# Optimization experiments

Measured on AMD Instinct MI355X. Metric: run time of the kernel, lower is better.

## Reference

```python
import jax, jax.numpy as jnp
import numpy as np

HID = 512
HEADS = 8
HD = HID // HEADS  # 64


def setup_inputs() -> dict:
    key = jax.random.key(0)
    ks = jax.random.split(key, 16)
    B, LQ, LK = 2, 384, 384
    s_in = 1.0 / np.sqrt(HID)
    s_hd = 1.0 / np.sqrt(HD)
    return {
        "query": jax.random.normal(ks[0], (B, LQ, HID), jnp.float32),
        "key":   jax.random.normal(ks[1], (B, LK, HID), jnp.float32),
        "value": jax.random.normal(ks[2], (B, LK, HID), jnp.float32),
        # linear weights stored as (in, out) so y = x @ W + b
        "Wq": jax.random.uniform(ks[3], (HID, HID), jnp.float32, -s_in, s_in),
        "bq": jnp.zeros((HID,), jnp.float32),
        "Wk": jax.random.uniform(ks[4], (HID, HID), jnp.float32, -s_in, s_in),
        "bk": jnp.zeros((HID,), jnp.float32),
        "Wv": jax.random.uniform(ks[5], (HID, HID), jnp.float32, -s_in, s_in),
        "bv": jnp.zeros((HID,), jnp.float32),
        "Ww": jax.random.uniform(ks[6], (HD, HD), jnp.float32, -s_hd, s_hd),
        "bw": jnp.zeros((HD,), jnp.float32),
        "Wu": jax.random.uniform(ks[7], (HD, HD), jnp.float32, -s_hd, s_hd),
        "bu": jnp.zeros((HD,), jnp.float32),
        "vv": jax.random.uniform(ks[8], (HD,), jnp.float32, -s_hd, s_hd),
        "Wo": jax.random.uniform(ks[9], (HID, HID), jnp.float32, -s_in, s_in),
        "bo": jnp.zeros((HID,), jnp.float32),
    }


def reference(query, key, value, Wq, bq, Wk, bk, Wv, bv, Ww, bw, Wu, bu, vv, Wo, bo):
    B, LQ, _ = query.shape
    LK = key.shape[1]
    scale = jnp.sqrt(jnp.asarray(HD, query.dtype))

    def split_heads(x, L):
        return x.reshape(B, L, HEADS, HD).transpose(0, 2, 1, 3)  # [B,H,L,hd]

    Q = split_heads(query @ Wq + bq, LQ)
    K = split_heads(key @ Wk + bk, LK)
    V = split_heads(value @ Wv + bv, LK)

    qW = Q @ Ww + bw            # [B,H,Lq,hd]
    kU = K @ Wu + bu            # [B,H,Lk,hd]
    # additive energy: tanh(W(Q)+U(K)) . vv  -> [B,H,Lq,Lk]
    e = jnp.tanh(qW[:, :, :, None, :] + kU[:, :, None, :, :])  # [B,H,Lq,Lk,hd]
    energy = jnp.einsum('bhqkd,d->bhqk', e, vv) / scale

    attention = jax.nn.softmax(energy, axis=-1)
    x = jnp.einsum('bhqk,bhkd->bhqd', attention, V)
    x = x.transpose(0, 2, 1, 3).reshape(B, LQ, HID)
    x = x @ Wo + bo
    return (x, attention)
```

## Files before the change

kernel.cpp:

```cpp
#include <hip/hip_runtime.h>

#define HID 512
#define HEADS 8
#define HD 64
#define BATCH 2
#define SEQ 384
#define MROWS (BATCH * SEQ)
#define APACK_S8 (48 * 32 * 64)
#define BPACK_S8 (32 * 32 * 64)

#define C1 2.8853900817779268f
#define SSCL 0.18033688011112043f

typedef __attribute__((ext_vector_type(8))) short s8v;
typedef __attribute__((ext_vector_type(4))) float f4v;

__device__ __forceinline__ unsigned short bf16_rne(float x) {
    union { float f; unsigned u; } v; v.f = x;
    unsigned r = v.u + 0x7FFFu + ((v.u >> 16) & 1u);
    return (unsigned short)(r >> 16);
}
__device__ __forceinline__ float bf16_val(unsigned short h) {
    union { float f; unsigned u; } v; v.u = ((unsigned)h) << 16; return v.f;
}

__device__ __forceinline__ void pack_a_one(const float* __restrict__ src,
                                           s8v* __restrict__ dst, int rem)
{
    int g = rem & 63, m = rem >> 6;
    const float4* sp = (const float4*)(src + (size_t)m * HID + g * 8);
    float4 v0 = sp[0], v1 = sp[1];
    float vals[8] = {v0.x, v0.y, v0.z, v0.w, v1.x, v1.y, v1.z, v1.w};
    s8v hi, lo;
    #pragma unroll
    for (int j = 0; j < 8; ++j) {
        unsigned short h = bf16_rne(vals[j]);
        hi[j] = (short)h;
        lo[j] = (short)bf16_rne(vals[j] - bf16_val(h));
    }
    int mt = m >> 4, kt = g >> 2;
    int lanei = (m & 15) | ((g & 3) << 4);
    size_t base = ((size_t)mt * 32) * 64 + lanei;
    dst[base + (size_t)kt * 64]        = hi;
    dst[base + (size_t)(16 + kt) * 64] = lo;
}

__device__ __forceinline__ void pack_w_store(s8v* __restrict__ dst,
                                             const float vals[8], int kg, int n)
{
    s8v hi, lo;
    #pragma unroll
    for (int j = 0; j < 8; ++j) {
        unsigned short h = bf16_rne(vals[j]);
        hi[j] = (short)h;
        lo[j] = (short)bf16_rne(vals[j] - bf16_val(h));
    }
    int nt = n >> 4, kt = kg >> 2;
    int lanei = (n & 15) | ((kg & 3) << 4);
    size_t base = ((size_t)nt * 32) * 64 + lanei;
    dst[base + (size_t)kt * 64]        = hi;
    dst[base + (size_t)(16 + kt) * 64] = lo;
}

__device__ __forceinline__ void pack_w_one(const float* __restrict__ W,
                                           s8v* __restrict__ dst, int rem)
{
    int kg = rem >> 9, n = rem & 511;
    float vals[8];
    #pragma unroll
    for (int j = 0; j < 8; ++j)
        vals[j] = W[(size_t)(kg * 8 + j) * HID + n];
    pack_w_store(dst, vals, kg, n);
}

__device__ __forceinline__ void fold_pack_w_one(const float* __restrict__ Wbig,
                                                const float* __restrict__ Wsmall,
                                                s8v* __restrict__ dst, int rem)
{
    int kg = __builtin_amdgcn_readfirstlane(rem >> 9);
    int n  = rem & 511;
    int h  = __builtin_amdgcn_readfirstlane(n >> 6);
    int d  = n & 63;
    const float* wr = Wbig + (size_t)(kg * 8) * HID + h * HD;
    float acc[8] = {0.f, 0.f, 0.f, 0.f, 0.f, 0.f, 0.f, 0.f};
    #pragma unroll 8
    for (int t = 0; t < 64; ++t) {
        float wv = Wsmall[t * 64 + d];
        #pragma unroll
        for (int j = 0; j < 8; ++j)
            acc[j] = fmaf(wr[(size_t)j * HID + t], wv, acc[j]);
    }
    pack_w_store(dst, acc, kg, n);
}

__global__ __launch_bounds__(256) void pack_all_kernel(
    const float* __restrict__ q, const float* __restrict__ k, const float* __restrict__ v,
    const float* __restrict__ Wq, const float* __restrict__ bq,
    const float* __restrict__ Wk, const float* __restrict__ bk,
    const float* __restrict__ Wv, const float* __restrict__ Wo,
    const float* __restrict__ Ww, const float* __restrict__ bw,
    const float* __restrict__ Wu, const float* __restrict__ bu,
    const float* __restrict__ vv,
    s8v* __restrict__ Aq, s8v* __restrict__ Ak, s8v* __restrict__ Av,
    s8v* __restrict__ Bq, s8v* __restrict__ Bk, s8v* __restrict__ Bv, s8v* __restrict__ Bo,
    float* __restrict__ bqe, float* __restrict__ bke, float* __restrict__ vv2)
{
    int bx = blockIdx.x, tid = threadIdx.x;
    if (bx < 576) {
        int p = bx / 192;
        int rem = (bx % 192) * 256 + tid;
        const float* src = (p == 0) ? q : (p == 1) ? k : v;
        s8v* dst = (p == 0) ? Aq : (p == 1) ? Ak : Av;
        pack_a_one(src, dst, rem);
    } else if (bx < 704) {
        pack_w_one(Wv, Bv, (bx - 576) * 256 + tid);
    } else if (bx < 832) {
        pack_w_one(Wo, Bo, (bx - 704) * 256 + tid);
    } else if (bx < 960) {
        fold_pack_w_one(Wq, Ww, Bq, (bx - 832) * 256 + tid);
    } else if (bx < 1088) {
        fold_pack_w_one(Wk, Wu, Bk, (bx - 960) * 256 + tid);
    } else {
        for (int i = tid; i < 1088; i += 256) {
            if (i < 512) {
                int h = i >> 6, j = i & 63;
                float s = bw[j];
                for (int t = 0; t < 64; ++t) s = fmaf(bq[h * 64 + t], Ww[t * 64 + j], s);
                bqe[i] = s;
            } else if (i < 1024) {
                int n = i - 512, h = n >> 6, j = n & 63;
                float s = bu[j];
                for (int t = 0; t < 64; ++t) s = fmaf(bk[h * 64 + t], Wu[t * 64 + j], s);
                bke[n] = s;
            } else {
                vv2[i - 1024] = -2.0f * vv[i - 1024];
            }
        }
    }
}

struct Frag { s8v ah0, al0, ah1, al1, bh0, bl0, bh1, bl1; };

__device__ __forceinline__ void load_frag(Frag& f,
    const s8v* __restrict__ a0, const s8v* __restrict__ a1,
    const s8v* __restrict__ b0, const s8v* __restrict__ b1, int kt)
{
    int oh = kt * 64, ol = (16 + kt) * 64;
    f.ah0 = a0[oh]; f.al0 = a0[ol];
    f.ah1 = a1[oh]; f.al1 = a1[ol];
    f.bh0 = b0[oh]; f.bl0 = b0[ol];
    f.bh1 = b1[oh]; f.bl1 = b1[ol];
}

__device__ __forceinline__ void compute_frag(f4v& acc00, f4v& acc01,
                                             f4v& acc10, f4v& acc11, const Frag& f)
{
    acc00 = __builtin_amdgcn_mfma_f32_16x16x32_bf16(f.ah0, f.bh0, acc00, 0, 0, 0);
    acc01 = __builtin_amdgcn_mfma_f32_16x16x32_bf16(f.ah0, f.bh1, acc01, 0, 0, 0);
    acc10 = __builtin_amdgcn_mfma_f32_16x16x32_bf16(f.ah1, f.bh0, acc10, 0, 0, 0);
    acc11 = __builtin_amdgcn_mfma_f32_16x16x32_bf16(f.ah1, f.bh1, acc11, 0, 0, 0);
    acc00 = __builtin_amdgcn_mfma_f32_16x16x32_bf16(f.ah0, f.bl0, acc00, 0, 0, 0);
    acc01 = __builtin_amdgcn_mfma_f32_16x16x32_bf16(f.ah0, f.bl1, acc01, 0, 0, 0);
    acc10 = __builtin_amdgcn_mfma_f32_16x16x32_bf16(f.ah1, f.bl0, acc10, 0, 0, 0);
    acc11 = __builtin_amdgcn_mfma_f32_16x16x32_bf16(f.ah1, f.bl1, acc11, 0, 0, 0);
    acc00 = __builtin_amdgcn_mfma_f32_16x16x32_bf16(f.al0, f.bh0, acc00, 0, 0, 0);
    acc01 = __builtin_amdgcn_mfma_f32_16x16x32_bf16(f.al0, f.bh1, acc01, 0, 0, 0);
    acc10 = __builtin_amdgcn_mfma_f32_16x16x32_bf16(f.al1, f.bh0, acc10, 0, 0, 0);
    acc11 = __builtin_amdgcn_mfma_f32_16x16x32_bf16(f.al1, f.bh1, acc11, 0, 0, 0);
}

template <int MODE>
__device__ __forceinline__ void mfma_gemm_body(
    const s8v* __restrict__ Ap, const s8v* __restrict__ Bp,
    const float* __restrict__ bias, float* __restrict__ out,
    int mt0, int nt0)
{
    __shared__ f4v red[4][4][64];

    int tid  = threadIdx.x;
    int wave = __builtin_amdgcn_readfirstlane(tid >> 6);
    int lane = tid & 63;

    const s8v* a0p = Ap + (size_t)(mt0 * 32) * 64 + lane;
    const s8v* a1p = a0p + (size_t)32 * 64;
    const s8v* b0p = Bp + (size_t)(nt0 * 32) * 64 + lane;
    const s8v* b1p = b0p + (size_t)32 * 64;

    f4v acc00 = {0.f, 0.f, 0.f, 0.f};
    f4v acc01 = {0.f, 0.f, 0.f, 0.f};
    f4v acc10 = {0.f, 0.f, 0.f, 0.f};
    f4v acc11 = {0.f, 0.f, 0.f, 0.f};

    int kt0 = wave * 4;
    Frag X, Y;
    load_frag(X, a0p, a1p, b0p, b1p, kt0);
    load_frag(Y, a0p, a1p, b0p, b1p, kt0 + 1);
    compute_frag(acc00, acc01, acc10, acc11, X);
    load_frag(X, a0p, a1p, b0p, b1p, kt0 + 2);
    compute_frag(acc00, acc01, acc10, acc11, Y);
    load_frag(Y, a0p, a1p, b0p, b1p, kt0 + 3);
    compute_frag(acc00, acc01, acc10, acc11, X);
    compute_frag(acc00, acc01, acc10, acc11, Y);

    red[wave][0][lane] = acc00;
    red[wave][1][lane] = acc01;
    red[wave][2][lane] = acc10;
    red[wave][3][lane] = acc11;
    __syncthreads();

    f4v s = red[0][wave][lane] + red[1][wave][lane]
          + red[2][wave][lane] + red[3][wave][lane];

    int quad = lane >> 4, c16 = lane & 15;
    int R0 = mt0 * 16 + quad * 4 + (wave >> 1) * 16;
    int C  = nt0 * 16 + c16 + (wave & 1) * 16;
    float biasC = bias[C];

    #pragma unroll
    for (int r = 0; r < 4; ++r) {
        float yy = s[r] + biasC;
        if (MODE != 0) yy = __builtin_amdgcn_exp2f(C1 * yy);
        if (MODE == 2) {
            int ROW = R0 + r;
            int b2 = ROW / SEQ, kk = ROW - b2 * SEQ;
            int hh = C >> 6, dd = C & 63;
            out[(((size_t)((b2 * 8 + hh) * 16 + (dd >> 2)) * SEQ + kk) << 2)
                + (dd & 3)] = yy;
        } else {
            out[(size_t)(R0 + r) * HID + C] = yy;
        }
    }
}

__global__ __launch_bounds__(256) void proj3_mfma_kernel(
    const s8v* __restrict__ Aq, const s8v* __restrict__ Ak, const s8v* __restrict__ Av,
    const s8v* __restrict__ Bq, const s8v* __restrict__ Bk, const s8v* __restrict__ Bv,
    const float* __restrict__ bqe, const float* __restrict__ bke, const float* __restrict__ bv,
    float* __restrict__ Eq, float* __restrict__ Ek4, float* __restrict__ V)
{
    int p = blockIdx.z;
    int mt0 = blockIdx.x * 2, nt0 = blockIdx.y * 2;
    if (p == 0)      mfma_gemm_body<1>(Aq, Bq, bqe, Eq,  mt0, nt0);
    else if (p == 1) mfma_gemm_body<2>(Ak, Bk, bke, Ek4, mt0, nt0);
    else             mfma_gemm_body<0>(Av, Bv, bv,  V,   mt0, nt0);
}

__global__ __launch_bounds__(256) void out_mfma_kernel(
    const s8v* __restrict__ Ax, const s8v* __restrict__ Bo,
    const float* __restrict__ bo, float* __restrict__ out)
{
    mfma_gemm_body<0>(Ax, Bo, bo, out, blockIdx.x * 2, blockIdx.y * 2);
}

__global__ __launch_bounds__(256, 4) void attn_kernel(
    const float* __restrict__ Eq, const float* __restrict__ Ek4,
    const float* __restrict__ V, const float* __restrict__ vv2,
    float* __restrict__ attnOut, s8v* __restrict__ Ax)
{
    __shared__ float2 aP[4][SEQ];

    int blk = blockIdx.x;
    int xcd = blk & 7, slot = blk >> 3;
    int part = slot / 48, qblk = slot % 48;
    int bh = xcd * 2 + part;
    int b = bh >> 3, h = bh & 7;
    int tid = threadIdx.x;
    int wave = __builtin_amdgcn_readfirstlane(tid >> 6);
    int lane = tid & 63;
    int q0 = qblk * 8 + wave * 2, q1 = q0 + 1;

    const float* eq0 = Eq + (size_t)(b * SEQ + q0) * HID + h * HD;
    const float* eq1 = eq0 + HID;
    const float4* ekbase = (const float4*)Ek4 + (size_t)bh * 16 * SEQ + lane;

    float e0[6], e1[6];
    #pragma unroll
    for (int t = 0; t < 6; ++t) { e0[t] = 0.f; e1[t] = 0.f; }

    #pragma unroll 1
    for (int cc = 0; cc < 4; ++cc) {
        int c = (cc + wave) & 3;
        float g0[16], g1[16], w[16];
        #pragma unroll
        for (int j = 0; j < 16; ++j) {
            g0[j] = eq0[c * 16 + j];
            g1[j] = eq1[c * 16 + j];
            w[j]  = vv2[c * 16 + j];
        }
        const float4* ekc = ekbase + (size_t)c * 4 * SEQ;
        float4 k0 = ekc[0 * SEQ], k1 = ekc[1 * SEQ];
        float4 k2 = ekc[2 * SEQ], k3 = ekc[3 * SEQ];
        #pragma unroll
        for (int kt = 0; kt < 6; ++kt) {
            float4 n0, n1, n2, n3;
            if (kt < 5) {
                const float4* np = ekc + (kt + 1) * 64;
                n0 = np[0 * SEQ]; n1 = np[1 * SEQ];
                n2 = np[2 * SEQ]; n3 = np[3 * SEQ];
            }
            float r0 = e0[kt], r1 = e1[kt];
            #define EN(J, KV)                                                      \
            {                                                                      \
                float t0 = __builtin_amdgcn_rcpf(fmaf(g0[J], (KV), 1.f));          \
                float t1 = __builtin_amdgcn_rcpf(fmaf(g1[J], (KV), 1.f));          \
                r0 = fmaf(w[J], t0, r0);                                           \
                r1 = fmaf(w[J], t1, r1);                                           \
            }
            EN(0,  k0.x) EN(1,  k0.y) EN(2,  k0.z) EN(3,  k0.w)
            EN(4,  k1.x) EN(5,  k1.y) EN(6,  k1.z) EN(7,  k1.w)
            EN(8,  k2.x) EN(9,  k2.y) EN(10, k2.z) EN(11, k2.w)
            EN(12, k3.x) EN(13, k3.y) EN(14, k3.z) EN(15, k3.w)
            #undef EN
            e0[kt] = r0; e1[kt] = r1;
            k0 = n0; k1 = n1; k2 = n2; k3 = n3;
        }
    }

    int ko = lane >> 4, d4p = lane & 15;
    const float4* vb = (const float4*)&V[(size_t)b * SEQ * HID + h * HD + d4p * 4];
    float4 vpre[8];
    #pragma unroll
    for (int i = 0; i < 8; ++i)
        vpre[i] = vb[(size_t)(ko + i * 4) * (HID / 4)];

    float m0 = e0[0], m1 = e1[0];
    #pragma unroll
    for (int t = 1; t < 6; ++t) { m0 = fmaxf(m0, e0[t]); m1 = fmaxf(m1, e1[t]); }
    #pragma unroll
    for (int off = 1; off < 64; off <<= 1) {
        m0 = fmaxf(m0, __shfl_xor(m0, off));
        m1 = fmaxf(m1, __shfl_xor(m1, off));
    }
    float a0[6], a1[6], s0 = 0.f, s1 = 0.f;
    #pragma unroll
    for (int t = 0; t < 6; ++t) {
        a0[t] = __builtin_amdgcn_exp2f((e0[t] - m0) * SSCL); s0 += a0[t];
        a1[t] = __builtin_amdgcn_exp2f((e1[t] - m1) * SSCL); s1 += a1[t];
    }
    #pragma unroll
    for (int off = 1; off < 64; off <<= 1) {
        s0 += __shfl_xor(s0, off);
        s1 += __shfl_xor(s1, off);
    }
    float z0 = __builtin_amdgcn_rcpf(s0), z1 = __builtin_amdgcn_rcpf(s1);

    size_t abase = (size_t)bh * SEQ * SEQ + (size_t)q0 * SEQ;
    #pragma unroll
    for (int t = 0; t < 6; ++t) {
        float v0 = a0[t] * z0, v1 = a1[t] * z1;
        attnOut[abase + t * 64 + lane] = v0;
        attnOut[abase + SEQ + t * 64 + lane] = v1;
        aP[wave][t * 64 + lane] = make_float2(v0, v1);
    }

    float4 x0 = make_float4(0.f, 0.f, 0.f, 0.f);
    float4 x1 = make_float4(0.f, 0.f, 0.f, 0.f);
    #pragma unroll
    for (int i = 0; i < 8; ++i) {
        int k = ko + i * 4;
        float4 v = vpre[i];
        float2 a = aP[wave][k];
        x0.x = fmaf(a.x, v.x, x0.x); x0.y = fmaf(a.x, v.y, x0.y);
        x0.z = fmaf(a.x, v.z, x0.z); x0.w = fmaf(a.x, v.w, x0.w);
        x1.x = fmaf(a.y, v.x, x1.x); x1.y = fmaf(a.y, v.y, x1.y);
        x1.z = fmaf(a.y, v.z, x1.z); x1.w = fmaf(a.y, v.w, x1.w);
    }
    #pragma unroll 8
    for (int k = ko + 32; k < SEQ; k += 4) {
        float4 v = vb[(size_t)k * (HID / 4)];
        float2 a = aP[wave][k];
        x0.x = fmaf(a.x, v.x, x0.x); x0.y = fmaf(a.x, v.y, x0.y);
        x0.z = fmaf(a.x, v.z, x0.z); x0.w = fmaf(a.x, v.w, x0.w);
        x1.x = fmaf(a.y, v.x, x1.x); x1.y = fmaf(a.y, v.y, x1.y);
        x1.z = fmaf(a.y, v.z, x1.z); x1.w = fmaf(a.y, v.w, x1.w);
    }
    #pragma unroll
    for (int off = 16; off < 64; off <<= 1) {
        x0.x += __shfl_xor(x0.x, off); x0.y += __shfl_xor(x0.y, off);
        x0.z += __shfl_xor(x0.z, off); x0.w += __shfl_xor(x0.w, off);
        x1.x += __shfl_xor(x1.x, off); x1.y += __shfl_xor(x1.y, off);
        x1.z += __shfl_xor(x1.z, off); x1.w += __shfl_xor(x1.w, off);
    }

    if (ko == 0) {
        float4 p0, p1;
        p0.x = __shfl_xor(x0.x, 1); p0.y = __shfl_xor(x0.y, 1);
        p0.z = __shfl_xor(x0.z, 1); p0.w = __shfl_xor(x0.w, 1);
        p1.x = __shfl_xor(x1.x, 1); p1.y = __shfl_xor(x1.y, 1);
        p1.z = __shfl_xor(x1.z, 1); p1.w = __shfl_xor(x1.w, 1);
        float vals[8];
        int row;
        if ((lane & 1) == 0) {
            vals[0] = x0.x; vals[1] = x0.y; vals[2] = x0.z; vals[3] = x0.w;
            vals[4] = p0.x; vals[5] = p0.y; vals[6] = p0.z; vals[7] = p0.w;
            row = b * SEQ + q0;
        } else {
            vals[0] = p1.x; vals[1] = p1.y; vals[2] = p1.z; vals[3] = p1.w;
            vals[4] = x1.x; vals[5] = x1.y; vals[6] = x1.z; vals[7] = x1.w;
            row = b * SEQ + q1;
        }
        int g = h * 8 + (lane >> 1);
        s8v hi, lo;
        #pragma unroll
        for (int j = 0; j < 8; ++j) {
            unsigned short hh = bf16_rne(vals[j]);
            hi[j] = (short)hh;
            lo[j] = (short)bf16_rne(vals[j] - bf16_val(hh));
        }
        int mt = row >> 4, kt2 = g >> 2;
        int lanei = (row & 15) | ((g & 3) << 4);
        size_t base = ((size_t)mt * 32) * 64 + lanei;
        Ax[base + (size_t)kt2 * 64]        = hi;
        Ax[base + (size_t)(16 + kt2) * 64] = lo;
    }
}

extern "C" void kernel_launch(void* const* d_in, const int* in_sizes, int n_in,
                              void* d_out, int out_size, void* d_ws, size_t ws_size,
                              hipStream_t stream)
{
    const float* query = (const float*)d_in[0];
    const float* key   = (const float*)d_in[1];
    const float* value = (const float*)d_in[2];
    const float* Wq = (const float*)d_in[3];
    const float* bq = (const float*)d_in[4];
    const float* Wk = (const float*)d_in[5];
    const float* bk = (const float*)d_in[6];
    const float* Wv = (const float*)d_in[7];
    const float* bv = (const float*)d_in[8];
    const float* Ww = (const float*)d_in[9];
    const float* bw = (const float*)d_in[10];
    const float* Wu = (const float*)d_in[11];
    const float* bu = (const float*)d_in[12];
    const float* vv = (const float*)d_in[13];
    const float* Wo = (const float*)d_in[14];
    const float* bo = (const float*)d_in[15];

    float* out_x    = (float*)d_out;
    float* out_attn = out_x + (size_t)MROWS * HID;

    float* ws  = (float*)d_ws;
    float* bqe = ws;
    float* bke = bqe + 512;
    float* vv2 = bke + 512;
    float* EqB = vv2 + 64;
    float* Ek4 = EqB + 393216;
    float* Vw  = Ek4 + 393216;

    s8v* packs = (s8v*)(Vw + 393216);
    s8v* Aq = packs;
    s8v* Ak = Aq + APACK_S8;
    s8v* Av = Ak + APACK_S8;
    s8v* Ax = Av + APACK_S8;
    s8v* Bq = Ax + APACK_S8;
    s8v* Bk = Bq + BPACK_S8;
    s8v* Bv = Bk + BPACK_S8;
    s8v* Bo = Bv + BPACK_S8;

    pack_all_kernel<<<dim3(1089), 256, 0, stream>>>(
        query, key, value,
        Wq, bq, Wk, bk, Wv, Wo, Ww, bw, Wu, bu, vv,
        Aq, Ak, Av, Bq, Bk, Bv, Bo,
        bqe, bke, vv2);
    proj3_mfma_kernel<<<dim3(24, 16, 3), 256, 0, stream>>>(Aq, Ak, Av, Bq, Bk, Bv,
                                                           bqe, bke, bv,
                                                           EqB, Ek4, Vw);
    attn_kernel<<<dim3(768), 256, 0, stream>>>(EqB, Ek4, Vw, vv2, out_attn, Ax);
    out_mfma_kernel<<<dim3(24, 16), 256, 0, stream>>>(Ax, Bo, bo, out_x);
}
```

Measured before the change: 140.8 us.

## Stage Ek and V tiles through shared memory with register double-buffering in attention

The attention kernel now cooperatively loads each chunk of the projected keys into a block-wide shared-memory buffer, so the four waves reuse one copy instead of each wave fetching the same Ek data from global memory. The next chunk is prefetched into registers while the current one is consumed. The P·V stage gets the same treatment, with V tiles of 64 keys staged in shared memory. This cuts redundant global traffic but adds many __syncthreads barriers and 24KB of LDS per block, and the occupancy hint drops from 4 to 3 blocks per SIMD.

```diff
diff --git a/kernel.cpp b/kernel.cpp
--- a/kernel.cpp
+++ b/kernel.cpp
@@ -252,11 +252,12 @@
     mfma_gemm_body<0>(Ax, Bo, bo, out, blockIdx.x * 2, blockIdx.y * 2);
 }
 
-__global__ __launch_bounds__(256, 4) void attn_kernel(
+__global__ __launch_bounds__(256, 3) void attn_kernel(
     const float* __restrict__ Eq, const float* __restrict__ Ek4,
     const float* __restrict__ V, const float* __restrict__ vv2,
     float* __restrict__ attnOut, s8v* __restrict__ Ax)
 {
+    __shared__ float4 shbuf[4 * SEQ];
     __shared__ float2 aP[4][SEQ];
 
     int blk = blockIdx.x;
@@ -271,15 +272,26 @@
 
     const float* eq0 = Eq + (size_t)(b * SEQ + q0) * HID + h * HD;
     const float* eq1 = eq0 + HID;
-    const float4* ekbase = (const float4*)Ek4 + (size_t)bh * 16 * SEQ + lane;
+    const float4* ek4g = (const float4*)Ek4 + (size_t)bh * 16 * SEQ;
 
     float e0[6], e1[6];
     #pragma unroll
     for (int t = 0; t < 6; ++t) { e0[t] = 0.f; e1[t] = 0.f; }
 
+    float4 st[6];
+    #pragma unroll
+    for (int r = 0; r < 6; ++r) st[r] = ek4g[tid + r * 256];
+    #pragma unroll
+    for (int r = 0; r < 6; ++r) shbuf[tid + r * 256] = st[r];
+    __syncthreads();
+
     #pragma unroll 1
-    for (int cc = 0; cc < 4; ++cc) {
-        int c = (cc + wave) & 3;
+    for (int c = 0; c < 4; ++c) {
+        if (c < 3) {
+            const float4* src = ek4g + (size_t)(c + 1) * 4 * SEQ;
+            #pragma unroll
+            for (int r = 0; r < 6; ++r) st[r] = src[tid + r * 256];
+        }
         float g0[16], g1[16], w[16];
         #pragma unroll
         for (int j = 0; j < 16; ++j) {
@@ -287,17 +299,12 @@
             g1[j] = eq1[c * 16 + j];
             w[j]  = vv2[c * 16 + j];
         }
-        const float4* ekc = ekbase + (size_t)c * 4 * SEQ;
-        float4 k0 = ekc[0 * SEQ], k1 = ekc[1 * SEQ];
-        float4 k2 = ekc[2 * SEQ], k3 = ekc[3 * SEQ];
         #pragma unroll
         for (int kt = 0; kt < 6; ++kt) {
-            float4 n0, n1, n2, n3;
-            if (kt < 5) {
-                const float4* np = ekc + (kt + 1) * 64;
-                n0 = np[0 * SEQ]; n1 = np[1 * SEQ];
-                n2 = np[2 * SEQ]; n3 = np[3 * SEQ];
-            }
+            float4 k0 = shbuf[0 * SEQ + kt * 64 + lane];
+            float4 k1 = shbuf[1 * SEQ + kt * 64 + lane];
+            float4 k2 = shbuf[2 * SEQ + kt * 64 + lane];
+            float4 k3 = shbuf[3 * SEQ + kt * 64 + lane];
             float r0 = e0[kt], r1 = e1[kt];
             #define EN(J, KV)                                                      \
             {                                                                      \
@@ -312,16 +319,23 @@
             EN(12, k3.x) EN(13, k3.y) EN(14, k3.z) EN(15, k3.w)
             #undef EN
             e0[kt] = r0; e1[kt] = r1;
-            k0 = n0; k1 = n1; k2 = n2; k3 = n3;
+        }
+        if (c < 3) {
+            __syncthreads();
+            #pragma unroll
+            for (int r = 0; r < 6; ++r) shbuf[tid + r * 256] = st[r];
+            __syncthreads();
         }
     }
 
     int ko = lane >> 4, d4p = lane & 15;
-    const float4* vb = (const float4*)&V[(size_t)b * SEQ * HID + h * HD + d4p * 4];
-    float4 vpre[8];
-    #pragma unroll
-    for (int i = 0; i < 8; ++i)
-        vpre[i] = vb[(size_t)(ko + i * 4) * (HID / 4)];
+    const float4* vtg = (const float4*)V + (size_t)b * SEQ * (HID / 4) + h * 16;
+    float4 vt[4];
+    #pragma unroll
+    for (int r = 0; r < 4; ++r) {
+        int idx = tid + r * 256;
+        vt[r] = vtg[(size_t)(idx >> 4) * (HID / 4) + (idx & 15)];
+    }
 
     float m0 = e0[0], m1 = e1[0];
     #pragma unroll
@@ -353,26 +367,38 @@
         aP[wave][t * 64 + lane] = make_float2(v0, v1);
     }
 
+    __syncthreads();
+    #pragma unroll
+    for (int r = 0; r < 4; ++r) shbuf[tid + r * 256] = vt[r];
+    __syncthreads();
+
     float4 x0 = make_float4(0.f, 0.f, 0.f, 0.f);
     float4 x1 = make_float4(0.f, 0.f, 0.f, 0.f);
-    #pragma unroll
-    for (int i = 0; i < 8; ++i) {
-        int k = ko + i * 4;
-        float4 v = vpre[i];
-        float2 a = aP[wave][k];
-        x0.x = fmaf(a.x, v.x, x0.x); x0.y = fmaf(a.x, v.y, x0.y);
-        x0.z = fmaf(a.x, v.z, x0.z); x0.w = fmaf(a.x, v.w, x0.w);
-        x1.x = fmaf(a.y, v.x, x1.x); x1.y = fmaf(a.y, v.y, x1.y);
-        x1.z = fmaf(a.y, v.z, x1.z); x1.w = fmaf(a.y, v.w, x1.w);
-    }
-    #pragma unroll 8
-    for (int k = ko + 32; k < SEQ; k += 4) {
-        float4 v = vb[(size_t)k * (HID / 4)];
-        float2 a = aP[wave][k];
-        x0.x = fmaf(a.x, v.x, x0.x); x0.y = fmaf(a.x, v.y, x0.y);
-        x0.z = fmaf(a.x, v.z, x0.z); x0.w = fmaf(a.x, v.w, x0.w);
-        x1.x = fmaf(a.y, v.x, x1.x); x1.y = fmaf(a.y, v.y, x1.y);
-        x1.z = fmaf(a.y, v.z, x1.z); x1.w = fmaf(a.y, v.w, x1.w);
+    #pragma unroll 1
+    for (int t = 0; t < 6; ++t) {
+        if (t < 5) {
+            #pragma unroll
+            for (int r = 0; r < 4; ++r) {
+                int idx = tid + r * 256;
+                vt[r] = vtg[(size_t)((t + 1) * 64 + (idx >> 4)) * (HID / 4) + (idx & 15)];
+            }
+        }
+        #pragma unroll
+        for (int i = 0; i < 16; ++i) {
+            int kk = ko + i * 4;
+            float4 v = shbuf[kk * 16 + d4p];
+            float2 a = aP[wave][t * 64 + kk];
+            x0.x = fmaf(a.x, v.x, x0.x); x0.y = fmaf(a.x, v.y, x0.y);
+            x0.z = fmaf(a.x, v.z, x0.z); x0.w = fmaf(a.x, v.w, x0.w);
+            x1.x = fmaf(a.y, v.x, x1.x); x1.y = fmaf(a.y, v.y, x1.y);
+            x1.z = fmaf(a.y, v.z, x1.z); x1.w = fmaf(a.y, v.w, x1.w);
+        }
+        if (t < 5) {
+            __syncthreads();
+            #pragma unroll
+            for (int r = 0; r < 4; ++r) shbuf[tid + r * 256] = vt[r];
+            __syncthreads();
+        }
     }
     #pragma unroll
     for (int off = 16; off < 64; off <<= 1) {
```

After: 167.3 us. 1.19x slower.

## Split attention energy over head-dim chunks per wave with LDS reduction

Applied to the files above, without the earlier changes.

Each block now handles 4 query rows instead of 8. Each wave computes partial energies for all 4 rows over its own 16-wide slice of the head dimension, so every K element it loads feeds 4 queries and the per-wave 4-chunk loop goes away. Partial energies are reduced through shared memory, each wave then runs the softmax for one row, and the attention-times-V product is split across waves by key range and reduced through LDS. The grid doubles to 1536 blocks and occupancy drops to 3 blocks per SM, in exchange for more register pressure, extra LDS traffic and three block-wide barriers.

```diff
diff --git a/kernel.cpp b/kernel.cpp
--- a/kernel.cpp
+++ b/kernel.cpp
@@ -252,127 +252,147 @@
     mfma_gemm_body<0>(Ax, Bo, bo, out, blockIdx.x * 2, blockIdx.y * 2);
 }
 
-__global__ __launch_bounds__(256, 4) void attn_kernel(
+__global__ __launch_bounds__(256, 3) void attn_kernel(
     const float* __restrict__ Eq, const float* __restrict__ Ek4,
     const float* __restrict__ V, const float* __restrict__ vv2,
     float* __restrict__ attnOut, s8v* __restrict__ Ax)
 {
-    __shared__ float2 aP[4][SEQ];
+    __shared__ __align__(16) float epart[4][4][SEQ];
+    __shared__ float aP[4][SEQ];
 
     int blk = blockIdx.x;
     int xcd = blk & 7, slot = blk >> 3;
-    int part = slot / 48, qblk = slot % 48;
+    int part = slot / 96, qslot = slot % 96;
     int bh = xcd * 2 + part;
     int b = bh >> 3, h = bh & 7;
     int tid = threadIdx.x;
     int wave = __builtin_amdgcn_readfirstlane(tid >> 6);
     int lane = tid & 63;
-    int q0 = qblk * 8 + wave * 2, q1 = q0 + 1;
-
-    const float* eq0 = Eq + (size_t)(b * SEQ + q0) * HID + h * HD;
-    const float* eq1 = eq0 + HID;
-    const float4* ekbase = (const float4*)Ek4 + (size_t)bh * 16 * SEQ + lane;
-
-    float e0[6], e1[6];
-    #pragma unroll
-    for (int t = 0; t < 6; ++t) { e0[t] = 0.f; e1[t] = 0.f; }
-
-    #pragma unroll 1
-    for (int cc = 0; cc < 4; ++cc) {
-        int c = (cc + wave) & 3;
-        float g0[16], g1[16], w[16];
-        #pragma unroll
-        for (int j = 0; j < 16; ++j) {
-            g0[j] = eq0[c * 16 + j];
-            g1[j] = eq1[c * 16 + j];
-            w[j]  = vv2[c * 16 + j];
+    int q0 = qslot * 4;
+
+    const float* eqb = Eq + (size_t)(b * SEQ + q0) * HID + h * HD + wave * 16;
+    float g0[16], g1[16], g2[16], g3[16], w[16];
+    #pragma unroll
+    for (int j = 0; j < 16; ++j) {
+        g0[j] = eqb[j];
+        g1[j] = eqb[HID + j];
+        g2[j] = eqb[2 * HID + j];
+        g3[j] = eqb[3 * HID + j];
+        w[j]  = vv2[wave * 16 + j];
+    }
+    const float4* ekc = (const float4*)Ek4 + (size_t)bh * 16 * SEQ
+                      + (size_t)wave * 4 * SEQ + lane;
+
+    float e0[6], e1[6], e2[6], e3[6];
+    #pragma unroll
+    for (int t = 0; t < 6; ++t) { e0[t] = 0.f; e1[t] = 0.f; e2[t] = 0.f; e3[t] = 0.f; }
+
+    float4 k0 = ekc[0 * SEQ], k1 = ekc[1 * SEQ];
+    float4 k2 = ekc[2 * SEQ], k3 = ekc[3 * SEQ];
+    #pragma unroll
+    for (int kt = 0; kt < 6; ++kt) {
+        float4 n0, n1, n2, n3;
+        if (kt < 5) {
+            const float4* np = ekc + (kt + 1) * 64;
+            n0 = np[0 * SEQ]; n1 = np[1 * SEQ];
+            n2 = np[2 * SEQ]; n3 = np[3 * SEQ];
         }
-        const float4* ekc = ekbase + (size_t)c * 4 * SEQ;
-        float4 k0 = ekc[0 * SEQ], k1 = ekc[1 * SEQ];
-        float4 k2 = ekc[2 * SEQ], k3 = ekc[3 * SEQ];
-        #pragma unroll
-        for (int kt = 0; kt < 6; ++kt) {
-            float4 n0, n1, n2, n3;
-            if (kt < 5) {
-                const float4* np = ekc + (kt + 1) * 64;
-                n0 = np[0 * SEQ]; n1 = np[1 * SEQ];
-                n2 = np[2 * SEQ]; n3 = np[3 * SEQ];
-            }
-            float r0 = e0[kt], r1 = e1[kt];
-            #define EN(J, KV)                                                      \
-            {                                                                      \
-                float t0 = __builtin_amdgcn_rcpf(fmaf(g0[J], (KV), 1.f));          \
-                float t1 = __builtin_amdgcn_rcpf(fmaf(g1[J], (KV), 1.f));          \
-                r0 = fmaf(w[J], t0, r0);                                           \
-                r1 = fmaf(w[J], t1, r1);                                           \
-            }
-            EN(0,  k0.x) EN(1,  k0.y) EN(2,  k0.z) EN(3,  k0.w)
-            EN(4,  k1.x) EN(5,  k1.y) EN(6,  k1.z) EN(7,  k1.w)
-            EN(8,  k2.x) EN(9,  k2.y) EN(10, k2.z) EN(11, k2.w)
-            EN(12, k3.x) EN(13, k3.y) EN(14, k3.z) EN(15, k3.w)
-            #undef EN
-            e0[kt] = r0; e1[kt] = r1;
-            k0 = n0; k1 = n1; k2 = n2; k3 = n3;
+        float r0 = e0[kt], r1 = e1[kt], r2 = e2[kt], r3 = e3[kt];
+        #define EN(J, KV)                                                      \
+        {                                                                      \
+            float t0 = __builtin_amdgcn_rcpf(fmaf(g0[J], (KV), 1.f));          \
+            float t1 = __builtin_amdgcn_rcpf(fmaf(g1[J], (KV), 1.f));          \
+            float t2 = __builtin_amdgcn_rcpf(fmaf(g2[J], (KV), 1.f));          \
+            float t3 = __builtin_amdgcn_rcpf(fmaf(g3[J], (KV), 1.f));          \
+            r0 = fmaf(w[J], t0, r0);                                           \
+            r1 = fmaf(w[J], t1, r1);                                           \
+            r2 = fmaf(w[J], t2, r2);                                           \
+            r3 = fmaf(w[J], t3, r3);                                           \
         }
-    }
+        EN(0,  k0.x) EN(1,  k0.y) EN(2,  k0.z) EN(3,  k0.w)
+        EN(4,  k1.x) EN(5,  k1.y) EN(6,  k1.z) EN(7,  k1.w)
+        EN(8,  k2.x) EN(9,  k2.y) EN(10, k2.z) EN(11, k2.w)
+        EN(12, k3.x) EN(13, k3.y) EN(14, k3.z) EN(15, k3.w)
+        #undef EN
+        e0[kt] = r0; e1[kt] = r1; e2[kt] = r2; e3[kt] = r3;
+        k0 = n0; k1 = n1; k2 = n2; k3 = n3;
+    }
+
+    #pragma unroll
+    for (int t = 0; t < 6; ++t) {
+        epart[wave][0][t * 64 + lane] = e0[t];
+        epart[wave][1][t * 64 + lane] = e1[t];
+        epart[wave][2][t * 64 + lane] = e2[t];
+        epart[wave][3][t * 64 + lane] = e3[t];
+    }
+    __syncthreads();
 
     int ko = lane >> 4, d4p = lane & 15;
-    const float4* vb = (const float4*)&V[(size_t)b * SEQ * HID + h * HD + d4p * 4];
+    const float4* vb = (const float4*)V + (size_t)(b * SEQ) * (HID / 4) + h * 16 + d4p;
     float4 vpre[8];
     #pragma unroll
     for (int i = 0; i < 8; ++i)
-        vpre[i] = vb[(size_t)(ko + i * 4) * (HID / 4)];
-
-    float m0 = e0[0], m1 = e1[0];
-    #pragma unroll
-    for (int t = 1; t < 6; ++t) { m0 = fmaxf(m0, e0[t]); m1 = fmaxf(m1, e1[t]); }
-    #pragma unroll
-    for (int off = 1; off < 64; off <<= 1) {
-        m0 = fmaxf(m0, __shfl_xor(m0, off));
-        m1 = fmaxf(m1, __shfl_xor(m1, off));
-    }
-    float a0[6], a1[6], s0 = 0.f, s1 = 0.f;
+        vpre[i] = vb[(size_t)(96 * wave + i * 4 + ko) * (HID / 4)];
+
+    float e[6];
+    #pragma unroll
+    for (int t = 0; t < 6; ++t)
+        e[t] = (epart[0][wave][t * 64 + lane] + epart[1][wave][t * 64 + lane])
+             + (epart[2][wave][t * 64 + lane] + epart[3][wave][t * 64 + lane]);
+    float m = e[0];
+    #pragma unroll
+    for (int t = 1; t < 6; ++t) m = fmaxf(m, e[t]);
+    #pragma unroll
+    for (int off = 1; off < 64; off <<= 1) m = fmaxf(m, __shfl_xor(m, off));
+    float a[6], s = 0.f;
     #pragma unroll
     for (int t = 0; t < 6; ++t) {
-        a0[t] = __builtin_amdgcn_exp2f((e0[t] - m0) * SSCL); s0 += a0[t];
-        a1[t] = __builtin_amdgcn_exp2f((e1[t] - m1) * SSCL); s1 += a1[t];
-    }
-    #pragma unroll
-    for (int off = 1; off < 64; off <<= 1) {
-        s0 += __shfl_xor(s0, off);
-        s1 += __shfl_xor(s1, off);
-    }
-    float z0 = __builtin_amdgcn_rcpf(s0), z1 = __builtin_amdgcn_rcpf(s1);
-
-    size_t abase = (size_t)bh * SEQ * SEQ + (size_t)q0 * SEQ;
+        a[t] = __builtin_amdgcn_exp2f((e[t] - m) * SSCL); s += a[t];
+    }
+    #pragma unroll
+    for (int off = 1; off < 64; off <<= 1) s += __shfl_xor(s, off);
+    float z = __builtin_amdgcn_rcpf(s);
+
+    size_t abase = (size_t)bh * SEQ * SEQ + (size_t)(q0 + wave) * SEQ;
     #pragma unroll
     for (int t = 0; t < 6; ++t) {
-        float v0 = a0[t] * z0, v1 = a1[t] * z1;
-        attnOut[abase + t * 64 + lane] = v0;
-        attnOut[abase + SEQ + t * 64 + lane] = v1;
-        aP[wave][t * 64 + lane] = make_float2(v0, v1);
-    }
+        float av = a[t] * z;
+        attnOut[abase + t * 64 + lane] = av;
+        aP[wave][t * 64 + lane] = av;
+    }
+    __syncthreads();
 
     float4 x0 = make_float4(0.f, 0.f, 0.f, 0.f);
     float4 x1 = make_float4(0.f, 0.f, 0.f, 0.f);
+    float4 x2 = make_float4(0.f, 0.f, 0.f, 0.f);
+    float4 x3 = make_float4(0.f, 0.f, 0.f, 0.f);
     #pragma unroll
     for (int i = 0; i < 8; ++i) {
-        int k = ko + i * 4;
+        int k = 96 * wave + i * 4 + ko;
         float4 v = vpre[i];
-        float2 a = aP[wave][k];
-        x0.x = fmaf(a.x, v.x, x0.x); x0.y = fmaf(a.x, v.y, x0.y);
-        x0.z = fmaf(a.x, v.z, x0.z); x0.w = fmaf(a.x, v.w, x0.w);
-        x1.x = fmaf(a.y, v.x, x1.x); x1.y = fmaf(a.y, v.y, x1.y);
-        x1.z = fmaf(a.y, v.z, x1.z); x1.w = fmaf(a.y, v.w, x1.w);
-    }
-    #pragma unroll 8
-    for (int k = ko + 32; k < SEQ; k += 4) {
+        float a0 = aP[0][k], a1 = aP[1][k], a2 = aP[2][k], a3 = aP[3][k];
+        x0.x = fmaf(a0, v.x, x0.x); x0.y = fmaf(a0, v.y, x0.y);
+        x0.z = fmaf(a0, v.z, x0.z); x0.w = fmaf(a0, v.w, x0.w);
+        x1.x = fmaf(a1, v.x, x1.x); x1.y = fmaf(a1, v.y, x1.y);
+        x1.z = fmaf(a1, v.z, x1.z); x1.w = fmaf(a1, v.w, x1.w);
+        x2.x = fmaf(a2, v.x, x2.x); x2.y = fmaf(a2, v.y, x2.y);
+        x2.z = fmaf(a2, v.z, x2.z); x2.w = fmaf(a2, v.w, x2.w);
+        x3.x = fmaf(a3, v.x, x3.x); x3.y = fmaf(a3, v.y, x3.y);
+        x3.z = fmaf(a3, v.z, x3.z); x3.w = fmaf(a3, v.w, x3.w);
+    }
+    #pragma unroll
+    for (int i = 8; i < 24; ++i) {
+        int k = 96 * wave + i * 4 + ko;
         float4 v = vb[(size_t)k * (HID / 4)];
-        float2 a = aP[wave][k];
-        x0.x = fmaf(a.x, v.x, x0.x); x0.y = fmaf(a.x, v.y, x0.y);
-        x0.z = fmaf(a.x, v.z, x0.z); x0.w = fmaf(a.x, v.w, x0.w);
-        x1.x = fmaf(a.y, v.x, x1.x); x1.y = fmaf(a.y, v.y, x1.y);
-        x1.z = fmaf(a.y, v.z, x1.z); x1.w = fmaf(a.y, v.w, x1.w);
+        float a0 = aP[0][k], a1 = aP[1][k], a2 = aP[2][k], a3 = aP[3][k];
+        x0.x = fmaf(a0, v.x, x0.x); x0.y = fmaf(a0, v.y, x0.y);
+        x0.z = fmaf(a0, v.z, x0.z); x0.w = fmaf(a0, v.w, x0.w);
+        x1.x = fmaf(a1, v.x, x1.x); x1.y = fmaf(a1, v.y, x1.y);
+        x1.z = fmaf(a1, v.z, x1.z); x1.w = fmaf(a1, v.w, x1.w);
+        x2.x = fmaf(a2, v.x, x2.x); x2.y = fmaf(a2, v.y, x2.y);
+        x2.z = fmaf(a2, v.z, x2.z); x2.w = fmaf(a2, v.w, x2.w);
+        x3.x = fmaf(a3, v.x, x3.x); x3.y = fmaf(a3, v.y, x3.y);
+        x3.z = fmaf(a3, v.z, x3.z); x3.w = fmaf(a3, v.w, x3.w);
     }
     #pragma unroll
     for (int off = 16; off < 64; off <<= 1) {
@@ -380,26 +400,39 @@
         x0.z += __shfl_xor(x0.z, off); x0.w += __shfl_xor(x0.w, off);
         x1.x += __shfl_xor(x1.x, off); x1.y += __shfl_xor(x1.y, off);
         x1.z += __shfl_xor(x1.z, off); x1.w += __shfl_xor(x1.w, off);
-    }
-
-    if (ko == 0) {
-        float4 p0, p1;
-        p0.x = __shfl_xor(x0.x, 1); p0.y = __shfl_xor(x0.y, 1);
-        p0.z = __shfl_xor(x0.z, 1); p0.w = __shfl_xor(x0.w, 1);
-        p1.x = __shfl_xor(x1.x, 1); p1.y = __shfl_xor(x1.y, 1);
-        p1.z = __shfl_xor(x1.z, 1); p1.w = __shfl_xor(x1.w, 1);
-        float vals[8];
-        int row;
-        if ((lane & 1) == 0) {
-            vals[0] = x0.x; vals[1] = x0.y; vals[2] = x0.z; vals[3] = x0.w;
-            vals[4] = p0.x; vals[5] = p0.y; vals[6] = p0.z; vals[7] = p0.w;
-            row = b * SEQ + q0;
-        } else {
-            vals[0] = p1.x; vals[1] = p1.y; vals[2] = p1.z; vals[3] = p1.w;
-            vals[4] = x1.x; vals[5] = x1.y; vals[6] = x1.z; vals[7] = x1.w;
-            row = b * SEQ + q1;
-        }
-        int g = h * 8 + (lane >> 1);
+        x2.x += __shfl_xor(x2.x, off); x2.y += __shfl_xor(x2.y, off);
+        x2.z += __shfl_xor(x2.z, off); x2.w += __shfl_xor(x2.w, off);
+        x3.x += __shfl_xor(x3.x, off); x3.y += __shfl_xor(x3.y, off);
+        x3.z += __shfl_xor(x3.z, off); x3.w += __shfl_xor(x3.w, off);
+    }
+    float4* xpart = (float4*)&epart[0][0][0];
+    if (lane < 16) {
+        xpart[(wave * 4 + 0) * 16 + d4p] = x0;
+        xpart[(wave * 4 + 1) * 16 + d4p] = x1;
+        xpart[(wave * 4 + 2) * 16 + d4p] = x2;
+        xpart[(wave * 4 + 3) * 16 + d4p] = x3;
+    }
+    __syncthreads();
+
+    float4 pa = xpart[(0 * 4 + wave) * 16 + d4p];
+    float4 pb = xpart[(1 * 4 + wave) * 16 + d4p];
+    float4 pc = xpart[(2 * 4 + wave) * 16 + d4p];
+    float4 pd = xpart[(3 * 4 + wave) * 16 + d4p];
+    float4 xs;
+    xs.x = (pa.x + pb.x) + (pc.x + pd.x);
+    xs.y = (pa.y + pb.y) + (pc.y + pd.y);
+    xs.z = (pa.z + pb.z) + (pc.z + pd.z);
+    xs.w = (pa.w + pb.w) + (pc.w + pd.w);
+
+    int u2 = (lane & 7) * 2;
+    float f0 = __shfl(xs.x, u2),     f1 = __shfl(xs.y, u2);
+    float f2 = __shfl(xs.z, u2),     f3 = __shfl(xs.w, u2);
+    float f4 = __shfl(xs.x, u2 + 1), f5 = __shfl(xs.y, u2 + 1);
+    float f6 = __shfl(xs.z, u2 + 1), f7 = __shfl(xs.w, u2 + 1);
+    if (lane < 8) {
+        float vals[8] = {f0, f1, f2, f3, f4, f5, f6, f7};
+        int row = b * SEQ + q0 + wave;
+        int g = h * 8 + lane;
         s8v hi, lo;
         #pragma unroll
         for (int j = 0; j < 8; ++j) {
@@ -465,6 +498,6 @@
     proj3_mfma_kernel<<<dim3(24, 16, 3), 256, 0, stream>>>(Aq, Ak, Av, Bq, Bk, Bv,
                                                            bqe, bke, bv,
                                                            EqB, Ek4, Vw);
-    attn_kernel<<<dim3(768), 256, 0, stream>>>(EqB, Ek4, Vw, vv2, out_attn, Ax);
+    attn_kernel<<<dim3(1536), 256, 0, stream>>>(EqB, Ek4, Vw, vv2, out_attn, Ax);
     out_mfma_kernel<<<dim3(24, 16), 256, 0, stream>>>(Ax, Bo, bo, out_x);
 }
```

Measured after the change: 142.5 us. Within noise of the previous version (+1.2%).

## Store exp-transformed K projection as fp16 and preload all K tiles per chunk

Applied to the files above, without the earlier changes.

The K projection output (exp2 of the scaled key energy term) is now written as fp16 in an 8-wide interleaved layout instead of fp32 in a 4-wide one, which halves the bytes the attention kernel streams for K. The attention kernel loads all six K tiles for a 16-dim chunk up front into registers and converts fp16 to fp32 in-register, replacing the rolling one-tile prefetch. Launch bounds drop from 4 to 3 blocks per CU to give room for the extra registers. The cost is lower occupancy, added conversion instructions, and reduced precision (plus possible fp16 overflow) in the exponentiated K values.

```diff
diff --git a/kernel.cpp b/kernel.cpp
--- a/kernel.cpp
+++ b/kernel.cpp
@@ -14,6 +14,7 @@
 
 typedef __attribute__((ext_vector_type(8))) short s8v;
 typedef __attribute__((ext_vector_type(4))) float f4v;
+typedef _Float16 h8v __attribute__((ext_vector_type(8)));
 
 __device__ __forceinline__ unsigned short bf16_rne(float x) {
     union { float f; unsigned u; } v; v.f = x;
@@ -224,8 +225,9 @@
             int ROW = R0 + r;
             int b2 = ROW / SEQ, kk = ROW - b2 * SEQ;
             int hh = C >> 6, dd = C & 63;
-            out[(((size_t)((b2 * 8 + hh) * 16 + (dd >> 2)) * SEQ + kk) << 2)
-                + (dd & 3)] = yy;
+            _Float16* o16 = (_Float16*)out;
+            o16[((size_t)((b2 * 8 + hh) * 8 + (dd >> 3)) * SEQ + kk) * 8
+                + (dd & 7)] = (_Float16)yy;
         } else {
             out[(size_t)(R0 + r) * HID + C] = yy;
         }
@@ -236,13 +238,13 @@
     const s8v* __restrict__ Aq, const s8v* __restrict__ Ak, const s8v* __restrict__ Av,
     const s8v* __restrict__ Bq, const s8v* __restrict__ Bk, const s8v* __restrict__ Bv,
     const float* __restrict__ bqe, const float* __restrict__ bke, const float* __restrict__ bv,
-    float* __restrict__ Eq, float* __restrict__ Ek4, float* __restrict__ V)
+    float* __restrict__ Eq, float* __restrict__ Ek16, float* __restrict__ V)
 {
     int p = blockIdx.z;
     int mt0 = blockIdx.x * 2, nt0 = blockIdx.y * 2;
-    if (p == 0)      mfma_gemm_body<1>(Aq, Bq, bqe, Eq,  mt0, nt0);
-    else if (p == 1) mfma_gemm_body<2>(Ak, Bk, bke, Ek4, mt0, nt0);
-    else             mfma_gemm_body<0>(Av, Bv, bv,  V,   mt0, nt0);
+    if (p == 0)      mfma_gemm_body<1>(Aq, Bq, bqe, Eq,   mt0, nt0);
+    else if (p == 1) mfma_gemm_body<2>(Ak, Bk, bke, Ek16, mt0, nt0);
+    else             mfma_gemm_body<0>(Av, Bv, bv,  V,    mt0, nt0);
 }
 
 __global__ __launch_bounds__(256) void out_mfma_kernel(
@@ -252,8 +254,8 @@
     mfma_gemm_body<0>(Ax, Bo, bo, out, blockIdx.x * 2, blockIdx.y * 2);
 }
 
-__global__ __launch_bounds__(256, 4) void attn_kernel(
-    const float* __restrict__ Eq, const float* __restrict__ Ek4,
+__global__ __launch_bounds__(256, 3) void attn_kernel(
+    const float* __restrict__ Eq, const _Float16* __restrict__ Ek16,
     const float* __restrict__ V, const float* __restrict__ vv2,
     float* __restrict__ attnOut, s8v* __restrict__ Ax)
 {
@@ -271,7 +273,7 @@
 
     const float* eq0 = Eq + (size_t)(b * SEQ + q0) * HID + h * HD;
     const float* eq1 = eq0 + HID;
-    const float4* ekbase = (const float4*)Ek4 + (size_t)bh * 16 * SEQ + lane;
+    const float4* ekf = (const float4*)Ek16 + (size_t)bh * 8 * SEQ + lane;
 
     float e0[6], e1[6];
     #pragma unroll
@@ -280,6 +282,12 @@
     #pragma unroll 1
     for (int cc = 0; cc < 4; ++cc) {
         int c = (cc + wave) & 3;
+        const float4* p0 = ekf + (size_t)(c * 2) * SEQ;
+        const float4* p1 = p0 + SEQ;
+        float4 L0[6], L1[6];
+        #pragma unroll
+        for (int kt = 0; kt < 6; ++kt) { L0[kt] = p0[kt * 64]; L1[kt] = p1[kt * 64]; }
+
         float g0[16], g1[16], w[16];
         #pragma unroll
         for (int j = 0; j < 16; ++j) {
@@ -287,32 +295,28 @@
             g1[j] = eq1[c * 16 + j];
             w[j]  = vv2[c * 16 + j];
         }
-        const float4* ekc = ekbase + (size_t)c * 4 * SEQ;
-        float4 k0 = ekc[0 * SEQ], k1 = ekc[1 * SEQ];
-        float4 k2 = ekc[2 * SEQ], k3 = ekc[3 * SEQ];
         #pragma unroll
         for (int kt = 0; kt < 6; ++kt) {
-            float4 n0, n1, n2, n3;
-            if (kt < 5) {
-                const float4* np = ekc + (kt + 1) * 64;
-                n0 = np[0 * SEQ]; n1 = np[1 * SEQ];
-                n2 = np[2 * SEQ]; n3 = np[3 * SEQ];
+            h8v ha = *(h8v*)&L0[kt];
+            h8v hb = *(h8v*)&L1[kt];
+            float kv[16];
+            #pragma unroll
+            for (int j = 0; j < 8; ++j) {
+                kv[j]     = (float)ha[j];
+                kv[8 + j] = (float)hb[j];
             }
             float r0 = e0[kt], r1 = e1[kt];
-            #define EN(J, KV)                                                      \
+            #define EN(J)                                                          \
             {                                                                      \
-                float t0 = __builtin_amdgcn_rcpf(fmaf(g0[J], (KV), 1.f));          \
-                float t1 = __builtin_amdgcn_rcpf(fmaf(g1[J], (KV), 1.f));          \
+                float t0 = __builtin_amdgcn_rcpf(fmaf(g0[J], kv[J], 1.f));         \
+                float t1 = __builtin_amdgcn_rcpf(fmaf(g1[J], kv[J], 1.f));         \
                 r0 = fmaf(w[J], t0, r0);                                           \
                 r1 = fmaf(w[J], t1, r1);                                           \
             }
-            EN(0,  k0.x) EN(1,  k0.y) EN(2,  k0.z) EN(3,  k0.w)
-            EN(4,  k1.x) EN(5,  k1.y) EN(6,  k1.z) EN(7,  k1.w)
-            EN(8,  k2.x) EN(9,  k2.y) EN(10, k2.z) EN(11, k2.w)
-            EN(12, k3.x) EN(13, k3.y) EN(14, k3.z) EN(15, k3.w)
+            EN(0)  EN(1)  EN(2)  EN(3)  EN(4)  EN(5)  EN(6)  EN(7)
+            EN(8)  EN(9)  EN(10) EN(11) EN(12) EN(13) EN(14) EN(15)
             #undef EN
             e0[kt] = r0; e1[kt] = r1;
-            k0 = n0; k1 = n1; k2 = n2; k3 = n3;
         }
     }
 
@@ -444,8 +448,8 @@
     float* bke = bqe + 512;
     float* vv2 = bke + 512;
     float* EqB = vv2 + 64;
-    float* Ek4 = EqB + 393216;
-    float* Vw  = Ek4 + 393216;
+    float* Ek16 = EqB + 393216;
+    float* Vw  = Ek16 + 393216;
 
     s8v* packs = (s8v*)(Vw + 393216);
     s8v* Aq = packs;
@@ -464,7 +468,8 @@
         bqe, bke, vv2);
     proj3_mfma_kernel<<<dim3(24, 16, 3), 256, 0, stream>>>(Aq, Ak, Av, Bq, Bk, Bv,
                                                            bqe, bke, bv,
-                                                           EqB, Ek4, Vw);
-    attn_kernel<<<dim3(768), 256, 0, stream>>>(EqB, Ek4, Vw, vv2, out_attn, Ax);
+                                                           EqB, Ek16, Vw);
+    attn_kernel<<<dim3(768), 256, 0, stream>>>(EqB, (const _Float16*)Ek16, Vw, vv2,
+                                               out_attn, Ax);
     out_mfma_kernel<<<dim3(24, 16), 256, 0, stream>>>(Ax, Bo, bo, out_x);
 }
```

Result: no change. 141.6 us (+0.5%).
